# Performance work log

Hardware: AMD Instinct MI355X
Metric: run time of the kernel (lower is better)

## Reference

```python
import jax, jax.numpy as jnp
import numpy as np

H = 800          # config.param.hidden_size (768 bert + 32 pos)
BERT_H = 768
POS_DIM = 32
NHEAD = 8
DH = 100         # gat_nhidden; NHEAD*DH == H
GAT_LAYERS = 2
N_EVENTS = 66
N_ROLES = 122
EPS = 0.1        # label smoothing
NEG_SLOPE = 0.2  # GATConv leaky_relu slope


def bilstm(x, Wih_f, Whh_f, b_f, Wih_b, Whh_b, b_b):
    """x: [B,T,D] -> [B,T,2H] (torch gate order i,f,g,o)."""
    def run(xs, Wih, Whh, b):
        B = xs.shape[1]; Hd = Whh.shape[1]
        def step(carry, xt):
            h, c = carry
            g = xt @ Wih.T + h @ Whh.T + b
            i, f, gg, o = jnp.split(g, 4, axis=-1)
            c = jax.nn.sigmoid(f) * c + jax.nn.sigmoid(i) * jnp.tanh(gg)
            h = jax.nn.sigmoid(o) * jnp.tanh(c)
            return (h, c), h
        init = (jnp.zeros((B, Hd), xs.dtype), jnp.zeros((B, Hd), xs.dtype))
        _, hs = jax.lax.scan(step, init, xs)
        return hs
    xt = jnp.swapaxes(x, 0, 1)                      # [T,B,D]
    hf = run(xt, Wih_f, Whh_f, b_f)
    hb = run(xt[::-1], Wih_b, Whh_b, b_b)[::-1]
    return jnp.swapaxes(jnp.concatenate([hf, hb], -1), 0, 1)


def gat_conv(x, src, dst, W, a_src, a_dst, bias):
    """PyG GATConv, concat heads, with self-loops. x:[n,H], src/dst:[E]."""
    n = x.shape[0]
    loops = jnp.arange(n)
    s = jnp.concatenate([src, loops])
    d = jnp.concatenate([dst, loops])
    h = (x @ W).reshape(n, NHEAD, DH)
    a_s = jnp.einsum('nhd,hd->nh', h, a_src)
    a_d = jnp.einsum('nhd,hd->nh', h, a_dst)
    e = jax.nn.leaky_relu(a_s[s] + a_d[d], NEG_SLOPE)              # [E,nh]
    m = jnp.full((n, NHEAD), -jnp.inf, x.dtype).at[d].max(e)       # segment max
    ex = jnp.exp(e - m[d])
    den = jnp.zeros((n, NHEAD), x.dtype).at[d].add(ex)
    alpha = ex / den[d]
    out = jnp.zeros((n, NHEAD, DH), x.dtype).at[d].add(alpha[..., None] * h[s])
    return out.reshape(n, NHEAD * DH) + bias


def label_smooth_ce(logits, target):
    c = logits.shape[-1]
    logp = jax.nn.log_softmax(logits, axis=-1)
    smooth = -logp.sum(-1)
    nll = -jnp.take_along_axis(logp, target[..., None], axis=-1)[..., 0]
    return smooth * EPS / c + (1.0 - EPS) * nll


def setup_inputs() -> dict:
    key = jax.random.key(0)
    ks = iter(jax.random.split(key, 32))
    B, S, E = 4, 128, 256
    std = 0.02
    inp = {}
    inp['bert_out'] = jax.random.normal(next(ks), (B, S + 1, BERT_H), jnp.float32)
    inp['pos_ids'] = jax.random.randint(next(ks), (B, S), 0, 31)
    inp['edge_src'] = jax.random.randint(next(ks), (B, E), 0, S)
    inp['edge_dst'] = jax.random.randint(next(ks), (B, E), 0, S)
    inp['start_labels'] = jax.random.randint(next(ks), (B, S, S), 0, N_EVENTS)
    inp['end_labels'] = jax.random.randint(next(ks), (B, S, S), 0, N_EVENTS)
    # parameters
    inp['pos_table'] = std * jax.random.normal(next(ks), (31, POS_DIM), jnp.float32)
    for sfx in ('f', 'b'):
        inp[f'Wih_{sfx}'] = std * jax.random.normal(next(ks), (4 * H, H), jnp.float32)
        inp[f'Whh_{sfx}'] = std * jax.random.normal(next(ks), (4 * H, H), jnp.float32)
        inp[f'bl_{sfx}'] = jnp.zeros((4 * H,), jnp.float32)
    inp['lstm_fc_W'] = std * jax.random.normal(next(ks), (2 * H, H), jnp.float32)
    inp['lstm_fc_b'] = jnp.zeros((H,), jnp.float32)
    inp['table_W'] = std * jax.random.normal(next(ks), (2 * H, H), jnp.float32)
    inp['table_b'] = jnp.zeros((H,), jnp.float32)
    inp['gat_W'] = std * jax.random.normal(next(ks), (H, NHEAD * DH), jnp.float32)
    inp['gat_asrc'] = std * jax.random.normal(next(ks), (NHEAD, DH), jnp.float32)
    inp['gat_adst'] = std * jax.random.normal(next(ks), (NHEAD, DH), jnp.float32)
    inp['gat_bias'] = jnp.zeros((NHEAD * DH,), jnp.float32)
    inp['trig_W'] = std * jax.random.normal(next(ks), (H, N_EVENTS), jnp.float32)
    inp['trig_b'] = jnp.zeros((N_EVENTS,), jnp.float32)
    inp['rs_W'] = std * jax.random.normal(next(ks), (H, N_ROLES), jnp.float32)
    inp['rs_b'] = jnp.zeros((N_ROLES,), jnp.float32)
    inp['re_W'] = std * jax.random.normal(next(ks), (H, N_ROLES), jnp.float32)
    inp['re_b'] = jnp.zeros((N_ROLES,), jnp.float32)
    return inp


def reference(bert_out, pos_ids, edge_src, edge_dst, start_labels, end_labels,
              pos_table, Wih_f, Whh_f, bl_f, Wih_b, Whh_b, bl_b,
              lstm_fc_W, lstm_fc_b, table_W, table_b,
              gat_W, gat_asrc, gat_adst, gat_bias,
              trig_W, trig_b, rs_W, rs_b, re_W, re_b):
    B, S = pos_ids.shape
    # POS embedding, prepend zero vector for [CLS] position
    pos_emb = pos_table[pos_ids]                                   # [B,S,32]
    pos_emb = jnp.concatenate(
        [jnp.zeros((B, 1, POS_DIM), bert_out.dtype), pos_emb], axis=1)
    x = jnp.concatenate([bert_out, pos_emb], axis=-1)              # [B,S+1,800]
    lstm_out = bilstm(x, Wih_f, Whh_f, bl_f, Wih_b, Whh_b, bl_b)   # [B,S+1,1600]
    x = x + jax.nn.relu(lstm_out @ lstm_fc_W + lstm_fc_b)
    x = x[:, 1:, :]                                                # drop CLS -> [B,S,800]

    # per-sample residual GAT stack (eval mode: dropout is identity)
    def gat_stack(xi, si, di):
        for _ in range(GAT_LAYERS):
            xi = xi + jax.nn.relu(gat_conv(xi, si, di, gat_W, gat_asrc, gat_adst, gat_bias))
        return xi
    x = jax.vmap(gat_stack)(x, edge_src, edge_dst)                 # [B,S,800]

    # pairwise table: cat(x_i, x_j) -> fc -> gelu
    x1 = jnp.broadcast_to(x[:, :, None, :], (B, S, S, H))
    x2 = jnp.broadcast_to(x[:, None, :, :], (B, S, S, H))
    s_tab = jax.nn.gelu(jnp.concatenate([x1, x2], -1) @ table_W + table_b)  # [B,S,S,800]

    eye = jnp.eye(S, dtype=start_labels.dtype)
    trig_mask = eye                                                # [S,S]
    arg_mask = 1 - eye
    trig_maskf = trig_mask.astype(s_tab.dtype)
    arg_maskf = arg_mask.astype(s_tab.dtype)

    trig_logits = s_tab @ trig_W + trig_b                          # [B,S,S,66]
    arg1_logits = s_tab @ rs_W + rs_b                              # [B,S,S,122]
    arg2_logits = s_tab @ re_W + re_b

    def masked_mean(loss, maskf):
        return (loss * maskf).sum((1, 2)) / maskf.sum()

    l1 = masked_mean(label_smooth_ce(trig_logits, start_labels * trig_mask), trig_maskf)
    l2 = masked_mean(label_smooth_ce(arg1_logits, start_labels * arg_mask), arg_maskf)
    l3 = masked_mean(label_smooth_ce(arg2_logits, end_labels * arg_mask), arg_maskf)
    total_loss = (l1 + l2 + l3).sum()

    trig_pred = jnp.argmax(trig_logits, -1)
    a1_pred = jnp.argmax(arg1_logits + jnp.swapaxes(arg1_logits, 1, 2), -1)
    a2_pred = jnp.argmax(arg2_logits + jnp.swapaxes(arg2_logits, 1, 2), -1)
    results1 = trig_pred * trig_mask + a1_pred * arg_mask
    results2 = trig_pred * trig_mask + a2_pred * arg_mask
    return total_loss, results1, results2
```

## Files before the change

### kernel.cpp

```cpp
#include <hip/hip_runtime.h>
#include <hip/hip_bf16.h>

#define B4 4
#define S128 128
#define T129 129
#define H800 800
#define E256 256
#define NE 66
#define NR 122
#define DPW 8
#define NWGD 100

typedef float f32x4 __attribute__((ext_vector_type(4)));

#define HB_ROW 900

__device__ __forceinline__ float gelu_f(float x) {
    float t = 0.7978845608028654f * (x + 0.044715f * x * x * x);
    float e = __expf(2.f * t);
    float th = 1.f - 2.f / (e + 1.f);
    return 0.5f * x * (1.f + th);
}

__device__ __forceinline__ float embed_at(const float* __restrict__ bert,
                                          const int* __restrict__ pids,
                                          const float* __restrict__ ptab,
                                          int m, int c)
{
    if (c < 768) return bert[(size_t)m * 768 + c];
    int t = m % T129, b = m / T129;
    if (t == 0) return 0.f;
    return ptab[pids[b * S128 + t - 1] * 32 + (c - 768)];
}

template<int AMODE, int BTRANS, int EPI>
__global__ __launch_bounds__(256) void k_gemm(const float* __restrict__ A, const float* __restrict__ Bm,
                                              const float* __restrict__ bias, const float* __restrict__ res,
                                              float* __restrict__ C, int M, int N, int K)
{
    __shared__ float As[16][68];
    __shared__ float Bs[16][68];
    int m0 = blockIdx.x * 64, n0 = blockIdx.y * 64;
    int tid = threadIdx.x;
    int tm = tid & 15, tn = tid >> 4;
    int kkA = tid & 15, mmb = tid >> 4;
    int nnB = (tid & 15) * 4, kkB = tid >> 4;
    float acc[4][4] = {};
    float aP[4], bP[4];

    #pragma unroll
    for (int q = 0; q < 4; q++) {
        int m = m0 + mmb + q * 16;
        float v = 0.f;
        if (m < M) {
            int row = (AMODE == 1) ? (m + (m >> 7) + 1) : m;
            v = A[(size_t)row * K + kkA];
        }
        aP[q] = v;
    }
    if (BTRANS == 0) {
        int n = n0 + nnB;
        if (n + 3 < N) {
            float4 bv = *(const float4*)&Bm[(size_t)kkB * N + n];
            bP[0] = bv.x; bP[1] = bv.y; bP[2] = bv.z; bP[3] = bv.w;
        } else {
            #pragma unroll
            for (int q = 0; q < 4; q++)
                bP[q] = (n + q < N) ? Bm[(size_t)kkB * N + n + q] : 0.f;
        }
    } else {
        #pragma unroll
        for (int q = 0; q < 4; q++) {
            int n = n0 + mmb + q * 16;
            bP[q] = (n < N) ? Bm[(size_t)n * K + kkA] : 0.f;
        }
    }

    for (int k0 = 0; k0 < K; k0 += 16) {
        float aC[4], bC[4];
        #pragma unroll
        for (int q = 0; q < 4; q++) { aC[q] = aP[q]; bC[q] = bP[q]; }

        int kn = (k0 + 16 < K) ? (k0 + 16) : 0;
        #pragma unroll
        for (int q = 0; q < 4; q++) {
            int m = m0 + mmb + q * 16;
            float v = 0.f;
            if (m < M) {
                int row = (AMODE == 1) ? (m + (m >> 7) + 1) : m;
                v = A[(size_t)row * K + kn + kkA];
            }
            aP[q] = v;
        }
        if (BTRANS == 0) {
            int n = n0 + nnB;
            if (n + 3 < N) {
                float4 bv = *(const float4*)&Bm[(size_t)(kn + kkB) * N + n];
                bP[0] = bv.x; bP[1] = bv.y; bP[2] = bv.z; bP[3] = bv.w;
            } else {
                #pragma unroll
                for (int q = 0; q < 4; q++)
                    bP[q] = (n + q < N) ? Bm[(size_t)(kn + kkB) * N + n + q] : 0.f;
            }
        } else {
            #pragma unroll
            for (int q = 0; q < 4; q++) {
                int n = n0 + mmb + q * 16;
                bP[q] = (n < N) ? Bm[(size_t)n * K + kn + kkA] : 0.f;
            }
        }

        #pragma unroll
        for (int q = 0; q < 4; q++)
            As[kkA][mmb + q * 16] = aC[q];
        if (BTRANS == 0) {
            Bs[kkB][nnB + 0] = bC[0]; Bs[kkB][nnB + 1] = bC[1];
            Bs[kkB][nnB + 2] = bC[2]; Bs[kkB][nnB + 3] = bC[3];
        } else {
            #pragma unroll
            for (int q = 0; q < 4; q++)
                Bs[kkA][mmb + q * 16] = bC[q];
        }
        __syncthreads();
        #pragma unroll
        for (int kk = 0; kk < 16; kk++) {
            float4 a = *(const float4*)&As[kk][tm * 4];
            float4 bb = *(const float4*)&Bs[kk][tn * 4];
            float av[4] = {a.x, a.y, a.z, a.w};
            float bv[4] = {bb.x, bb.y, bb.z, bb.w};
            #pragma unroll
            for (int xx = 0; xx < 4; xx++)
                #pragma unroll
                for (int yy = 0; yy < 4; yy++)
                    acc[xx][yy] += av[xx] * bv[yy];
        }
        __syncthreads();
    }
    #pragma unroll
    for (int xx = 0; xx < 4; xx++) {
        int m = m0 + tm * 4 + xx;
        if (m >= M) continue;
        #pragma unroll
        for (int yy = 0; yy < 4; yy++) {
            int n = n0 + tn * 4 + yy;
            if (n >= N) continue;
            float v = acc[xx][yy];
            if (bias) v += bias[n];
            if (EPI == 1) v = res[(size_t)m * N + n] + fmaxf(v, 0.f);
            C[(size_t)m * N + n] = v;
        }
    }
}

__global__ __launch_bounds__(256) void k_gemm_wih(const float* __restrict__ bert,
                                                  const int* __restrict__ pids,
                                                  const float* __restrict__ ptab,
                                                  const float* __restrict__ Wf, const float* __restrict__ Wb,
                                                  const float* __restrict__ bf, const float* __restrict__ bb_,
                                                  float* __restrict__ C)
{
    __shared__ float As[16][68];
    __shared__ float Bs[16][68];
    const int M = 516, K = 800, N = 6400;
    int m0 = blockIdx.x * 64, n0 = blockIdx.y * 64;
    const float* W  = (n0 < 3200) ? Wf : Wb;
    const float* bi = (n0 < 3200) ? bf : bb_;
    int nb = (n0 < 3200) ? n0 : (n0 - 3200);
    int tid = threadIdx.x;
    int tm = tid & 15, tn = tid >> 4;
    int kk_s = tid & 15, mmb = tid >> 4;
    int mrow[4]; int pofs[4]; bool mok[4];
    #pragma unroll
    for (int q = 0; q < 4; q++) {
        int m = m0 + mmb + q * 16;
        mrow[q] = m;
        mok[q] = m < M;
        int t = m % T129, b = m / T129;
        pofs[q] = (mok[q] && t > 0) ? pids[b * S128 + t - 1] * 32 : -1;
    }
    float acc[4][4] = {};
    float aP[4], bP[4];

    #pragma unroll
    for (int q = 0; q < 4; q++) {
        float v = 0.f;
        if (mok[q]) {
            if (kk_s < 768) v = bert[(size_t)mrow[q] * 768 + kk_s];
            else            v = (pofs[q] < 0) ? 0.f : ptab[pofs[q] + kk_s - 768];
        }
        aP[q] = v;
    }
    #pragma unroll
    for (int q = 0; q < 4; q++)
        bP[q] = W[(size_t)(nb + mmb + q * 16) * K + kk_s];

    for (int k0 = 0; k0 < K; k0 += 16) {
        float aC[4], bC[4];
        #pragma unroll
        for (int q = 0; q < 4; q++) { aC[q] = aP[q]; bC[q] = bP[q]; }

        int kn = (k0 + 16 < K) ? (k0 + 16) : 0;
        {
            int c = kn + kk_s;
            #pragma unroll
            for (int q = 0; q < 4; q++) {
                float v = 0.f;
                if (mok[q]) {
                    if (c < 768) v = bert[(size_t)mrow[q] * 768 + c];
                    else         v = (pofs[q] < 0) ? 0.f : ptab[pofs[q] + c - 768];
                }
                aP[q] = v;
            }
        }
        #pragma unroll
        for (int q = 0; q < 4; q++)
            bP[q] = W[(size_t)(nb + mmb + q * 16) * K + kn + kk_s];

        #pragma unroll
        for (int q = 0; q < 4; q++)
            As[kk_s][mmb + q * 16] = aC[q];
        #pragma unroll
        for (int q = 0; q < 4; q++)
            Bs[kk_s][mmb + q * 16] = bC[q];
        __syncthreads();
        #pragma unroll
        for (int kk = 0; kk < 16; kk++) {
            float4 a = *(const float4*)&As[kk][tm * 4];
            float4 bb = *(const float4*)&Bs[kk][tn * 4];
            float av[4] = {a.x, a.y, a.z, a.w};
            float bv[4] = {bb.x, bb.y, bb.z, bb.w};
            #pragma unroll
            for (int xx = 0; xx < 4; xx++)
                #pragma unroll
                for (int yy = 0; yy < 4; yy++)
                    acc[xx][yy] += av[xx] * bv[yy];
        }
        __syncthreads();
    }
    #pragma unroll
    for (int xx = 0; xx < 4; xx++) {
        int m = m0 + tm * 4 + xx;
        if (m >= M) continue;
        #pragma unroll
        for (int yy = 0; yy < 4; yy++) {
            int n = n0 + tn * 4 + yy;
            C[(size_t)m * N + n] = acc[xx][yy] + bi[nb + (n - n0)];
        }
    }
}

__global__ __launch_bounds__(256) void k_gemm_fc(const float* __restrict__ A, const float* __restrict__ Bm,
                                                 const float* __restrict__ bias,
                                                 const float* __restrict__ bert, const int* __restrict__ pids,
                                                 const float* __restrict__ ptab, float* __restrict__ C)
{
    __shared__ float As[16][68];
    __shared__ float Bs[16][68];
    const int M = 516, N = 800, K = 1600;
    int m0 = blockIdx.x * 64, n0 = blockIdx.y * 64;
    int tid = threadIdx.x;
    int tm = tid & 15, tn = tid >> 4;
    int kkA = tid & 15, mmb = tid >> 4;
    int nnB = (tid & 15) * 4, kkB = tid >> 4;
    float acc[4][4] = {};
    float aP[4], bP[4];

    #pragma unroll
    for (int q = 0; q < 4; q++) {
        int m = m0 + mmb + q * 16;
        aP[q] = (m < M) ? A[(size_t)m * K + kkA] : 0.f;
    }
    {
        int n = n0 + nnB;
        if (n + 3 < N) {
            float4 bv = *(const float4*)&Bm[(size_t)kkB * N + n];
            bP[0] = bv.x; bP[1] = bv.y; bP[2] = bv.z; bP[3] = bv.w;
        } else {
            #pragma unroll
            for (int q = 0; q < 4; q++)
                bP[q] = (n + q < N) ? Bm[(size_t)kkB * N + n + q] : 0.f;
        }
    }

    for (int k0 = 0; k0 < K; k0 += 16) {
        float aC[4], bC[4];
        #pragma unroll
        for (int q = 0; q < 4; q++) { aC[q] = aP[q]; bC[q] = bP[q]; }

        int kn = (k0 + 16 < K) ? (k0 + 16) : 0;
        #pragma unroll
        for (int q = 0; q < 4; q++) {
            int m = m0 + mmb + q * 16;
            aP[q] = (m < M) ? A[(size_t)m * K + kn + kkA] : 0.f;
        }
        {
            int n = n0 + nnB;
            if (n + 3 < N) {
                float4 bv = *(const float4*)&Bm[(size_t)(kn + kkB) * N + n];
                bP[0] = bv.x; bP[1] = bv.y; bP[2] = bv.z; bP[3] = bv.w;
            } else {
                #pragma unroll
                for (int q = 0; q < 4; q++)
                    bP[q] = (n + q < N) ? Bm[(size_t)(kn + kkB) * N + n + q] : 0.f;
            }
        }

        #pragma unroll
        for (int q = 0; q < 4; q++)
            As[kkA][mmb + q * 16] = aC[q];
        Bs[kkB][nnB + 0] = bC[0]; Bs[kkB][nnB + 1] = bC[1];
        Bs[kkB][nnB + 2] = bC[2]; Bs[kkB][nnB + 3] = bC[3];
        __syncthreads();
        #pragma unroll
        for (int kk = 0; kk < 16; kk++) {
            float4 a = *(const float4*)&As[kk][tm * 4];
            float4 bb = *(const float4*)&Bs[kk][tn * 4];
            float av[4] = {a.x, a.y, a.z, a.w};
            float bv[4] = {bb.x, bb.y, bb.z, bb.w};
            #pragma unroll
            for (int xx = 0; xx < 4; xx++)
                #pragma unroll
                for (int yy = 0; yy < 4; yy++)
                    acc[xx][yy] += av[xx] * bv[yy];
        }
        __syncthreads();
    }
    #pragma unroll
    for (int xx = 0; xx < 4; xx++) {
        int m = m0 + tm * 4 + xx;
        if (m >= M) continue;
        #pragma unroll
        for (int yy = 0; yy < 4; yy++) {
            int n = n0 + tn * 4 + yy;
            if (n >= N) continue;
            float v = fmaxf(acc[xx][yy] + bias[n], 0.f);
            C[(size_t)m * N + n] = embed_at(bert, pids, ptab, m, n) + v;
        }
    }
}

__global__ __launch_bounds__(256) void k_gemm_uv(const float* __restrict__ A, const float* __restrict__ tW,
                                                 const float* __restrict__ tb, float* __restrict__ C)
{
    __shared__ float As[16][68];
    __shared__ float Bs[16][68];
    const int M = 512, K = 800, N = 1600;
    int m0 = blockIdx.x * 64, n0 = blockIdx.y * 64;
    int tid = threadIdx.x;
    int tm = tid & 15, tn = tid >> 4;
    int kkA = tid & 15, mmb = tid >> 4;
    int nnB = (tid & 15) * 4, kkB = tid >> 4;
    float acc[4][4] = {};
    float aP[4], bP[4];

    #pragma unroll
    for (int q = 0; q < 4; q++)
        aP[q] = A[(size_t)(m0 + mmb + q * 16) * K + kkA];
    #pragma unroll
    for (int q = 0; q < 4; q++) {
        int n = n0 + nnB + q;
        bP[q] = (n < 800) ? tW[(size_t)kkB * 800 + n]
                          : tW[(size_t)(800 + kkB) * 800 + (n - 800)];
    }

    for (int k0 = 0; k0 < K; k0 += 16) {
        float aC[4], bC[4];
        #pragma unroll
        for (int q = 0; q < 4; q++) { aC[q] = aP[q]; bC[q] = bP[q]; }

        int kn = (k0 + 16 < K) ? (k0 + 16) : 0;
        #pragma unroll
        for (int q = 0; q < 4; q++)
            aP[q] = A[(size_t)(m0 + mmb + q * 16) * K + kn + kkA];
        #pragma unroll
        for (int q = 0; q < 4; q++) {
            int n = n0 + nnB + q;
            bP[q] = (n < 800) ? tW[(size_t)(kn + kkB) * 800 + n]
                              : tW[(size_t)(800 + kn + kkB) * 800 + (n - 800)];
        }

        #pragma unroll
        for (int q = 0; q < 4; q++)
            As[kkA][mmb + q * 16] = aC[q];
        #pragma unroll
        for (int q = 0; q < 4; q++)
            Bs[kkB][nnB + q] = bC[q];
        __syncthreads();
        #pragma unroll
        for (int kk = 0; kk < 16; kk++) {
            float4 a = *(const float4*)&As[kk][tm * 4];
            float4 bb = *(const float4*)&Bs[kk][tn * 4];
            float av[4] = {a.x, a.y, a.z, a.w};
            float bv[4] = {bb.x, bb.y, bb.z, bb.w};
            #pragma unroll
            for (int xx = 0; xx < 4; xx++)
                #pragma unroll
                for (int yy = 0; yy < 4; yy++)
                    acc[xx][yy] += av[xx] * bv[yy];
        }
        __syncthreads();
    }
    #pragma unroll
    for (int xx = 0; xx < 4; xx++) {
        int m = m0 + tm * 4 + xx;
        #pragma unroll
        for (int yy = 0; yy < 4; yy++) {
            int n = n0 + tn * 4 + yy;
            float v = acc[xx][yy];
            if (n < 800) v += tb[n];
            C[(size_t)m * N + n] = v;
        }
    }
}

__global__ __launch_bounds__(256) void k_lstm(const float* __restrict__ xW,
                                              const float* __restrict__ Whhf, const float* __restrict__ Whhb,
                                              float* __restrict__ lstm, float* __restrict__ hpk)
{
    __shared__ float hb[4][HB_ROW];
    __shared__ float gsum[25][32][4];
    __shared__ float gg[128];
    int wg = blockIdx.x;
    int dir = wg >= NWGD ? 1 : 0;
    int wgd = dir ? wg - NWGD : wg;
    const float* Whh = dir ? Whhb : Whhf;
    const float* xWd = xW + dir * 3200;
    int tid = threadIdx.x;
    bool dotth = tid < 200;
    int d = tid & 7, sl = tid >> 3;
    int k0 = sl * 32;
    int rb = tid & 3, rd = (tid >> 2) & 7, rg = tid >> 5;
    int lane = tid & 63;

    float wreg[4][32];
    if (dotth) {
        #pragma unroll
        for (int g = 0; g < 4; g++) {
            const float* wp = Whh + (size_t)(g * 800 + wgd * DPW + d) * 800 + k0;
            #pragma unroll
            for (int q = 0; q < 32; q += 4)
                *(float4*)&wreg[g][q] = *(const float4*)&wp[q];
        }
    }
    for (int i = tid; i < 4 * HB_ROW; i += 256) (&hb[0][0])[i] = 0.f;
    __syncthreads();

    float cst = 0.f;

    for (int step = 0; step < 129; step++) {
        int t = dir ? (128 - step) : step;
        float xq = 0.f;
        if (tid < 128)
            xq = xWd[(size_t)(rb * T129 + t) * 6400 + rg * 800 + wgd * DPW + rd];
        if (step > 0) {
            int tprev = dir ? (t + 1) : (t - 1);
            if (tid < 200) {
                const f32x4* pb = (const f32x4*)(hpk + (size_t)(dir * 129 + tprev) * 3200);
                const f32x4* p0 = pb + tid;
                const f32x4* p1 = pb + tid + 200;
                const f32x4* p2 = pb + tid + 400;
                const f32x4* p3 = pb + tid + 600;
                f32x4 v0, v1, v2, v3;
                long long iters = 0;
                for (;;) {
                    asm volatile(
                        "global_load_dwordx4 %0, %4, off sc0 sc1\n\t"
                        "global_load_dwordx4 %1, %5, off sc0 sc1\n\t"
                        "global_load_dwordx4 %2, %6, off sc0 sc1\n\t"
                        "global_load_dwordx4 %3, %7, off sc0 sc1\n\t"
                        "s_waitcnt vmcnt(0)"
                        : "=&v"(v0), "=&v"(v1), "=&v"(v2), "=&v"(v3)
                        : "v"(p0), "v"(p1), "v"(p2), "v"(p3)
                        : "memory");
                    bool ok = fabsf(v0.x) < 1.5f && fabsf(v0.y) < 1.5f &&
                              fabsf(v0.z) < 1.5f && fabsf(v0.w) < 1.5f &&
                              fabsf(v1.x) < 1.5f && fabsf(v1.y) < 1.5f &&
                              fabsf(v1.z) < 1.5f && fabsf(v1.w) < 1.5f &&
                              fabsf(v2.x) < 1.5f && fabsf(v2.y) < 1.5f &&
                              fabsf(v2.z) < 1.5f && fabsf(v2.w) < 1.5f &&
                              fabsf(v3.x) < 1.5f && fabsf(v3.y) < 1.5f &&
                              fabsf(v3.z) < 1.5f && fabsf(v3.w) < 1.5f;
                    if (ok) break;
                    if (++iters > 20000000LL) break;
                }
                {
                    int s0 = tid;
                    int p_ = (s0 >> 3) * 8 + (s0 & 1) * 4;
                    ((f32x4*)&hb[0][0])[((s0 & 7) >> 1) * 225 + (p_ >> 5) * 9 + ((p_ & 31) >> 2)] = v0;
                }
                {
                    int s1 = tid + 200;
                    int p_ = (s1 >> 3) * 8 + (s1 & 1) * 4;
                    ((f32x4*)&hb[0][0])[((s1 & 7) >> 1) * 225 + (p_ >> 5) * 9 + ((p_ & 31) >> 2)] = v1;
                }
                {
                    int s2 = tid + 400;
                    int p_ = (s2 >> 3) * 8 + (s2 & 1) * 4;
                    ((f32x4*)&hb[0][0])[((s2 & 7) >> 1) * 225 + (p_ >> 5) * 9 + ((p_ & 31) >> 2)] = v2;
                }
                {
                    int s3 = tid + 600;
                    int p_ = (s3 >> 3) * 8 + (s3 & 1) * 4;
                    ((f32x4*)&hb[0][0])[((s3 & 7) >> 1) * 225 + (p_ >> 5) * 9 + ((p_ & 31) >> 2)] = v3;
                }
            }
            __syncthreads();
        }
        if (dotth) {
            float a[4][4] = {};
            #pragma unroll
            for (int b = 0; b < 4; b++) {
                const float* hrow = &hb[b][0];
                #pragma unroll
                for (int q = 0; q < 32; q += 4) {
                    float4 h = *(const float4*)&hrow[sl * 36 + q];
                    #pragma unroll
                    for (int g = 0; g < 4; g++)
                        a[g][b] += wreg[g][q] * h.x + wreg[g][q + 1] * h.y
                                 + wreg[g][q + 2] * h.z + wreg[g][q + 3] * h.w;
                }
            }
            #pragma unroll
            for (int g = 0; g < 4; g++)
                *(float4*)&gsum[sl][g * 8 + d][0] = make_float4(a[g][0], a[g][1], a[g][2], a[g][3]);
        }
        __syncthreads();
        if (tid < 128) {
            float s = xq;
            #pragma unroll
            for (int ss = 0; ss < 25; ss++) s += gsum[ss][rg * 8 + rd][rb];
            gg[tid] = s;
        }
        __syncthreads();
        float hv = 0.f;
        if (tid < 32) {
            int dd = tid & 7, bb2 = tid >> 3;
            float gi = gg[(0 << 5) | (dd << 2) | bb2];
            float gf = gg[(1 << 5) | (dd << 2) | bb2];
            float gG = gg[(2 << 5) | (dd << 2) | bb2];
            float go = gg[(3 << 5) | (dd << 2) | bb2];
            float si = 1.f / (1.f + __expf(-gi));
            float sf = 1.f / (1.f + __expf(-gf));
            float so = 1.f / (1.f + __expf(-go));
            cst = sf * cst + si * tanhf(gG);
            hv = so * tanhf(cst);
        }
        if (tid < 64) {
            int src = (lane & 7) * 4;
            f32x4 o;
            o.x = __shfl(hv, src + 0, 64);
            o.y = __shfl(hv, src + 1, 64);
            o.z = __shfl(hv, src + 2, 64);
            o.w = __shfl(hv, src + 3, 64);
            if (lane < 8) {
                float* pp = hpk + ((size_t)(dir * 129 + t) * 100 + wgd) * 32 + lane * 4;
                asm volatile("global_store_dwordx4 %0, %1, off sc0 sc1"
                             :: "v"((f32x4*)pp), "v"(o) : "memory");
            }
            if (lane < 8) {
                int bb = lane >> 1, half = lane & 1;
                float* ap = lstm + (size_t)((bb * T129 + t) * 1600) + dir * 800 + wgd * DPW + half * 4;
                asm volatile("global_store_dwordx4 %0, %1, off sc0 sc1"
                             :: "v"((f32x4*)ap), "v"(o) : "memory");
            }
        }
    }
}

template<int RESMODE>
__global__ __launch_bounds__(512) void k_gat_fused(const int* __restrict__ esrc, const int* __restrict__ edst,
                                                   const float* __restrict__ h1,
                                                   const float* __restrict__ asrc, const float* __restrict__ adst,
                                                   const float* __restrict__ gbias,
                                                   const float* __restrict__ res, float* __restrict__ out)
{
    __shared__ int se[384], de[384];
    __shared__ float asl[128], adl[128], ml[128], dl_[128];
    int bh = blockIdx.x;
    int b = bh >> 3, h = bh & 7;
    int t = threadIdx.x;
    if (t < 384) {
        if (t < E256) { se[t] = esrc[b * E256 + t]; de[t] = edst[b * E256 + t]; }
        else          { se[t] = t - E256;           de[t] = t - E256; }
    }
    int node = t >> 2, ch = t & 3;
    int dd0 = ch * 25;
    {
        const float* hp = h1 + (size_t)(b * S128 + node) * H800 + h * 100 + dd0;
        const float* ap = asrc + h * 100 + dd0;
        const float* dp = adst + h * 100 + dd0;
        float s1 = 0.f, s2 = 0.f;
        #pragma unroll
        for (int q = 0; q < 25; q++) { float hv = hp[q]; s1 += hv * ap[q]; s2 += hv * dp[q]; }
        s1 += __shfl_xor(s1, 1, 64); s1 += __shfl_xor(s1, 2, 64);
        s2 += __shfl_xor(s2, 1, 64); s2 += __shfl_xor(s2, 2, 64);
        if (ch == 0) { asl[node] = s1; adl[node] = s2; }
    }
    __syncthreads();
    if (t < 128) {
        float myad = adl[t];
        float m = -3.4e38f;
        for (int e = 0; e < 384; e++)
            if (de[e] == t) {
                float sc = asl[se[e]] + myad;
                sc = (sc > 0.f) ? sc : 0.2f * sc;
                m = fmaxf(m, sc);
            }
        float den = 0.f;
        for (int e = 0; e < 384; e++)
            if (de[e] == t) {
                float sc = asl[se[e]] + myad;
                sc = (sc > 0.f) ? sc : 0.2f * sc;
                den += __expf(sc - m);
            }
        ml[t] = m; dl_[t] = den;
    }
    __syncthreads();
    float acc[25] = {};
    float myad = adl[node], mym = ml[node];
    for (int e = 0; e < 384; e++) {
        if (de[e] == node) {
            int s = se[e];
            float sc = asl[s] + myad;
            sc = (sc > 0.f) ? sc : 0.2f * sc;
            float w = __expf(sc - mym);
            const float* hp = h1 + (size_t)(b * S128 + s) * H800 + h * 100 + dd0;
            #pragma unroll
            for (int q = 0; q < 25; q++) acc[q] += w * hp[q];
        }
    }
    float inv = 1.f / dl_[node];
    int n = b * S128 + node;
    size_t rrow = (RESMODE == 1) ? (size_t)(n + b + 1) * H800 : (size_t)n * H800;
    #pragma unroll
    for (int q = 0; q < 25; q++) {
        int col = h * 100 + dd0 + q;
        float v = acc[q] * inv + gbias[col];
        out[(size_t)n * H800 + col] = res[rrow + col] + fmaxf(v, 0.f);
    }
}

__global__ __launch_bounds__(64) void k_trig(const float* __restrict__ uv,
                                             const float* __restrict__ W, const float* __restrict__ bias,
                                             const int* __restrict__ labels, float* __restrict__ d_out)
{
    __shared__ float s[800];
    __shared__ float lg[66];
    int bi = blockIdx.x;
    int i = bi & 127;
    int l = threadIdx.x;
    const float* ur = uv + (size_t)bi * 1600;
    const float* vr = ur + 800;
    for (int k = l; k < 800; k += 64) s[k] = gelu_f(ur[k] + vr[k]);
    __syncthreads();
    float a0 = 0.f, a1 = 0.f;
    bool has2 = (l < 2);
    for (int k = 0; k < 800; k++) {
        float sv = s[k];
        a0 += sv * W[k * NE + l];
        if (has2) a1 += sv * W[k * NE + 64 + l];
    }
    lg[l] = a0 + bias[l];
    if (has2) lg[64 + l] = a1 + bias[64 + l];
    __syncthreads();
    if (l == 0) {
        float m = lg[0];
        for (int c = 1; c < NE; c++) m = fmaxf(m, lg[c]);
        float se = 0.f, sl = 0.f, bv = lg[0];
        int am = 0;
        for (int c = 0; c < NE; c++) {
            se += __expf(lg[c] - m);
            sl += lg[c];
            if (lg[c] > bv) { bv = lg[c]; am = c; }
        }
        float lse = m + __logf(se);
        int tgt = labels[(size_t)bi * S128 + i];
        float ce = (0.1f / NE) * (NE * lse - sl) + 0.9f * (lse - lg[tgt]);
        atomicAdd(d_out, ce * (1.f / 128.f));
        int r = bi * S128 + i;
        d_out[1 + r] = (float)am;
        d_out[1 + 65536 + r] = (float)am;
    }
}

__global__ __launch_bounds__(256) void k_logits2(const float* __restrict__ uvb,
                                                 const float* __restrict__ rsW, const float* __restrict__ rsb,
                                                 const float* __restrict__ reW, const float* __restrict__ reb,
                                                 float* __restrict__ L)
{
    __shared__ float As[16][68];
    __shared__ float Bs[16][256];
    int bi = blockIdx.y;
    const float* base = uvb + (size_t)bi * 128 * 1600;
    float* Lb = L + (size_t)bi * 16384 * 256;
    int il = blockIdx.x >> 1;
    int j0 = (blockIdx.x & 1) * 64;
    const float* urow = base + (size_t)il * 1600;
    int tid = threadIdx.x;
    int tm = tid & 7, tn = tid >> 3;
    float acc[8][8] = {};
    int ct = tid;
    int hc = (ct < 128) ? ct : (ct - 128);
    const float* Wp = (ct < 128) ? rsW : reW;
    bool cok = hc < NR;
    int kk = tid & 15, rrb = tid >> 4;

    float u_pf = urow[kk];
    float v_pf[4];
    #pragma unroll
    for (int q = 0; q < 4; q++)
        v_pf[q] = base[(size_t)(j0 + rrb + q * 16) * 1600 + 800 + kk];
    float w_pf[16];
    #pragma unroll
    for (int kk2 = 0; kk2 < 16; kk2++)
        w_pf[kk2] = cok ? Wp[(size_t)kk2 * NR + hc] : 0.f;

    for (int k0 = 0; k0 < 800; k0 += 16) {
        float u_cur = u_pf;
        float v_cur[4];
        #pragma unroll
        for (int q = 0; q < 4; q++) v_cur[q] = v_pf[q];
        float w_cur[16];
        #pragma unroll
        for (int kk2 = 0; kk2 < 16; kk2++) w_cur[kk2] = w_pf[kk2];

        int kn = (k0 + 16 < 800) ? (k0 + 16) : 0;
        u_pf = urow[kn + kk];
        #pragma unroll
        for (int q = 0; q < 4; q++)
            v_pf[q] = base[(size_t)(j0 + rrb + q * 16) * 1600 + 800 + kn + kk];
        #pragma unroll
        for (int kk2 = 0; kk2 < 16; kk2++)
            w_pf[kk2] = cok ? Wp[(size_t)(kn + kk2) * NR + hc] : 0.f;

        #pragma unroll
        for (int q = 0; q < 4; q++)
            As[kk][rrb + q * 16] = gelu_f(u_cur + v_cur[q]);
        #pragma unroll
        for (int kk2 = 0; kk2 < 16; kk2++)
            Bs[kk2][ct] = w_cur[kk2];
        __syncthreads();
        #pragma unroll
        for (int kki = 0; kki < 16; kki++) {
            float4 a0 = *(const float4*)&As[kki][tm * 8];
            float4 a1 = *(const float4*)&As[kki][tm * 8 + 4];
            float4 b0 = *(const float4*)&Bs[kki][tn * 8];
            float4 b1 = *(const float4*)&Bs[kki][tn * 8 + 4];
            float av[8] = {a0.x, a0.y, a0.z, a0.w, a1.x, a1.y, a1.z, a1.w};
            float bv[8] = {b0.x, b0.y, b0.z, b0.w, b1.x, b1.y, b1.z, b1.w};
            #pragma unroll
            for (int xx = 0; xx < 8; xx++)
                #pragma unroll
                for (int yy = 0; yy < 8; yy++)
                    acc[xx][yy] += av[xx] * bv[yy];
        }
        __syncthreads();
    }
    int head = tn >> 4;
    const float* bp = head ? reb : rsb;
    #pragma unroll
    for (int xx = 0; xx < 8; xx++) {
        int r = il * S128 + j0 + tm * 8 + xx;
        float* Lr = Lb + (size_t)r * 256 + tn * 8;
        #pragma unroll
        for (int hf = 0; hf < 2; hf++) {
            int c = (tn * 8 + hf * 4) & 127;
            if (c + 3 < NR) {
                float4 o = make_float4(acc[xx][hf*4+0] + bp[c+0], acc[xx][hf*4+1] + bp[c+1],
                                       acc[xx][hf*4+2] + bp[c+2], acc[xx][hf*4+3] + bp[c+3]);
                *(float4*)(Lr + hf * 4) = o;
            } else {
                #pragma unroll
                for (int q = 0; q < 4; q++)
                    if (c + q < NR) Lr[hf * 4 + q] = acc[xx][hf*4+q] + bp[c+q];
            }
        }
    }
}

__global__ __launch_bounds__(256) void k_loss2(const float* __restrict__ L,
                                               const int* __restrict__ lab0, const int* __restrict__ lab1,
                                               float* __restrict__ res0, float* __restrict__ res1,
                                               float* __restrict__ lossptr)
{
    __shared__ float wsum[4];
    int wv = threadIdx.x >> 6, l = threadIdx.x & 63;
    int rr = blockIdx.x * 4 + wv;
    int bi = rr >> 14;
    int r = rr & 16383;
    int i = r >> 7, j = r & 127;
    size_t bioff = (size_t)bi * 16384;
    float ces = 0.f;
    if (i != j) {
        const float* row  = L + (bioff + r) * 256;
        const float* prow = L + (bioff + ((j << 7) | i)) * 256;
        bool v2 = (l < NR - 64);
        #pragma unroll
        for (int hd = 0; hd < 2; hd++) {
            const float* rw = row + hd * 128;
            const float* pw = prow + hd * 128;
            float x1 = rw[l];
            float x2 = v2 ? rw[l + 64] : -3.4e38f;
            float m = fmaxf(x1, x2);
            #pragma unroll
            for (int s = 32; s; s >>= 1) m = fmaxf(m, __shfl_xor(m, s, 64));
            float se = __expf(x1 - m) + (v2 ? __expf(x2 - m) : 0.f);
            float sl = x1 + (v2 ? x2 : 0.f);
            #pragma unroll
            for (int s = 32; s; s >>= 1) { se += __shfl_xor(se, s, 64); sl += __shfl_xor(sl, s, 64); }
            float lse = m + __logf(se);
            int tgt = (hd ? lab1 : lab0)[bioff + r];
            float lt = rw[tgt];
            ces += (0.1f / NR) * (NR * lse - sl) + 0.9f * (lse - lt);
            float y1 = x1 + pw[l];
            float y2 = v2 ? (x2 + pw[l + 64]) : -3.4e38f;
            float bv; int bidx;
            if (y2 > y1) { bv = y2; bidx = l + 64; } else { bv = y1; bidx = l; }
            #pragma unroll
            for (int s = 32; s; s >>= 1) {
                float ov = __shfl_xor(bv, s, 64);
                int oi = __shfl_xor(bidx, s, 64);
                if (ov > bv || (ov == bv && oi < bidx)) { bv = ov; bidx = oi; }
            }
            if (l == 0) (hd ? res1 : res0)[bioff + r] = (float)bidx;
        }
    }
    if (l == 0) wsum[wv] = ces;
    __syncthreads();
    if (threadIdx.x == 0) {
        float s = (wsum[0] + wsum[1] + wsum[2] + wsum[3]) * (1.f / 16256.f);
        atomicAdd(lossptr, s);
    }
}

extern "C" void kernel_launch(void* const* d_in, const int* in_sizes, int n_in,
                              void* d_out, int out_size, void* d_ws, size_t ws_size,
                              hipStream_t stream)
{
    (void)in_sizes; (void)n_in; (void)out_size;
    const float* bert  = (const float*)d_in[0];
    const int*   pids  = (const int*)d_in[1];
    const int*   esrc  = (const int*)d_in[2];
    const int*   edst  = (const int*)d_in[3];
    const int*   slab  = (const int*)d_in[4];
    const int*   elab  = (const int*)d_in[5];
    const float* ptab  = (const float*)d_in[6];
    const float* Wih_f = (const float*)d_in[7];
    const float* Whh_f = (const float*)d_in[8];
    const float* bl_f  = (const float*)d_in[9];
    const float* Wih_b = (const float*)d_in[10];
    const float* Whh_b = (const float*)d_in[11];
    const float* bl_b  = (const float*)d_in[12];
    const float* fcW   = (const float*)d_in[13];
    const float* fcb   = (const float*)d_in[14];
    const float* tW    = (const float*)d_in[15];
    const float* tb    = (const float*)d_in[16];
    const float* gatW  = (const float*)d_in[17];
    const float* asrc  = (const float*)d_in[18];
    const float* adst  = (const float*)d_in[19];
    const float* gbias = (const float*)d_in[20];
    const float* trigW = (const float*)d_in[21];
    const float* trigb = (const float*)d_in[22];
    const float* rsW   = (const float*)d_in[23];
    const float* rsb   = (const float*)d_in[24];
    const float* reW   = (const float*)d_in[25];
    const float* reb   = (const float*)d_in[26];
    float* out = (float*)d_out;

    float* ws = (float*)d_ws;
    size_t off = 0;
    auto alloc = [&](size_t n) { float* p = ws + off; off += (n + 255) & ~(size_t)255; return p; };
    float* uv    = alloc((size_t)512 * 1600);
    float* R     = ws + off;
    size_t roff = 0;
    auto ralloc = [&](size_t n) { float* p = R + roff; roff += (n + 255) & ~(size_t)255; return p; };
    float* xW   = ralloc((size_t)516 * 6400);
    float* lstm = ralloc((size_t)516 * 1600);
    float* xg   = ralloc(516 * 800);
    float* h1   = ralloc(512 * 800);
    float* g1   = ralloc(512 * 800);
    float* g2   = ralloc(512 * 800);
    float* hpk  = ralloc((size_t)2 * 129 * 100 * 32);
    float* Lbuf = R;

    hipMemsetAsync(d_out, 0, 4, stream);
    hipMemsetAsync(hpk, 0x7F, (size_t)2 * 129 * 100 * 32 * sizeof(float), stream);

    k_gemm_wih<<<dim3(9, 100), 256, 0, stream>>>(bert, pids, ptab, Wih_f, Wih_b, bl_f, bl_b, xW);

    k_lstm<<<2 * NWGD, 256, 0, stream>>>(xW, Whh_f, Whh_b, lstm, hpk);

    k_gemm_fc<<<dim3(9, 13), 256, 0, stream>>>(lstm, fcW, fcb, bert, pids, ptab, xg);

    k_gemm<1, 0, 0><<<dim3(8, 13), 256, 0, stream>>>(xg, gatW, nullptr, nullptr, h1, 512, 800, 800);
    k_gat_fused<1><<<32, 512, 0, stream>>>(esrc, edst, h1, asrc, adst, gbias, xg, g1);
    k_gemm<0, 0, 0><<<dim3(8, 13), 256, 0, stream>>>(g1, gatW, nullptr, nullptr, h1, 512, 800, 800);
    k_gat_fused<0><<<32, 512, 0, stream>>>(esrc, edst, h1, asrc, adst, gbias, g1, g2);

    k_gemm_uv<<<dim3(8, 25), 256, 0, stream>>>(g2, tW, tb, uv);

    k_trig<<<512, 64, 0, stream>>>(uv, trigW, trigb, slab, out);

    size_t need4 = (off + (size_t)4 * 16384 * 256) * sizeof(float);
    if (ws_size >= need4) {
        k_logits2<<<dim3(256, 4), 256, 0, stream>>>(uv, rsW, rsb, reW, reb, Lbuf);
        k_loss2<<<16384, 256, 0, stream>>>(Lbuf, slab, elab,
                                           out + 1, out + 1 + 65536, out);
    } else {
        for (int bp = 0; bp < 2; bp++) {
            k_logits2<<<dim3(256, 2), 256, 0, stream>>>(uv + (size_t)bp * 2 * 128 * 1600,
                                                        rsW, rsb, reW, reb, Lbuf);
            k_loss2<<<8192, 256, 0, stream>>>(Lbuf,
                                              slab + (size_t)bp * 2 * 16384, elab + (size_t)bp * 2 * 16384,
                                              out + 1 + (size_t)bp * 2 * 16384,
                                              out + 1 + 65536 + (size_t)bp * 2 * 16384, out);
        }
    }
}
```

Before: 1.927 ms.

## Double-buffer GELU A tile and use per-wave weight tiles in logits2

```diff
diff --git a/kernel.cpp b/kernel.cpp
--- a/kernel.cpp
+++ b/kernel.cpp
@@ -688,8 +688,8 @@
                                                  const float* __restrict__ reW, const float* __restrict__ reb,
                                                  float* __restrict__ L)
 {
-    __shared__ float As[16][68];
-    __shared__ float Bs[16][256];
+    __shared__ float As[2][16][68];
+    __shared__ float Bs[4][16][68];
     int bi = blockIdx.y;
     const float* base = uvb + (size_t)bi * 128 * 1600;
     float* Lb = L + (size_t)bi * 16384 * 256;
@@ -697,62 +697,67 @@
     int j0 = (blockIdx.x & 1) * 64;
     const float* urow = base + (size_t)il * 1600;
     int tid = threadIdx.x;
+    int wv = tid >> 6, lane = tid & 63;
     int tm = tid & 7, tn = tid >> 3;
+    int cln = (tn & 7) * 8;
     float acc[8][8] = {};
-    int ct = tid;
-    int hc = (ct < 128) ? ct : (ct - 128);
-    const float* Wp = (ct < 128) ? rsW : reW;
+    int hc = (tid < 128) ? tid : (tid - 128);
+    const float* Wp = (tid < 128) ? rsW : reW;
     bool cok = hc < NR;
     int kk = tid & 15, rrb = tid >> 4;
 
-    float u_pf = urow[kk];
-    float v_pf[4];
+    float u0 = urow[kk];
+    float v0q[4];
     #pragma unroll
     for (int q = 0; q < 4; q++)
-        v_pf[q] = base[(size_t)(j0 + rrb + q * 16) * 1600 + 800 + kk];
-    float w_pf[16];
+        v0q[q] = base[(size_t)(j0 + rrb + q * 16) * 1600 + 800 + kk];
+    float wP[16];
     #pragma unroll
     for (int kk2 = 0; kk2 < 16; kk2++)
-        w_pf[kk2] = cok ? Wp[(size_t)kk2 * NR + hc] : 0.f;
-
-    for (int k0 = 0; k0 < 800; k0 += 16) {
-        float u_cur = u_pf;
-        float v_cur[4];
-        #pragma unroll
-        for (int q = 0; q < 4; q++) v_cur[q] = v_pf[q];
-        float w_cur[16];
-        #pragma unroll
-        for (int kk2 = 0; kk2 < 16; kk2++) w_cur[kk2] = w_pf[kk2];
-
-        int kn = (k0 + 16 < 800) ? (k0 + 16) : 0;
-        u_pf = urow[kn + kk];
+        wP[kk2] = cok ? Wp[(size_t)kk2 * NR + hc] : 0.f;
+    float uP = urow[16 + kk];
+    float vP[4];
+    #pragma unroll
+    for (int q = 0; q < 4; q++)
+        vP[q] = base[(size_t)(j0 + rrb + q * 16) * 1600 + 800 + 16 + kk];
+
+    #pragma unroll
+    for (int q = 0; q < 4; q++)
+        As[0][kk][rrb + q * 16] = gelu_f(u0 + v0q[q]);
+    __syncthreads();
+
+    for (int c = 0; c < 50; ++c) {
+        #pragma unroll
+        for (int kk2 = 0; kk2 < 16; kk2++)
+            Bs[wv][kk2][lane] = wP[kk2];
         #pragma unroll
         for (int q = 0; q < 4; q++)
-            v_pf[q] = base[(size_t)(j0 + rrb + q * 16) * 1600 + 800 + kn + kk];
+            As[(c + 1) & 1][kk][rrb + q * 16] = gelu_f(uP + vP[q]);
+
+        int k1 = (c + 1 < 50) ? (c + 1) * 16 : 0;
+        int k2 = (c + 2 < 50) ? (c + 2) * 16 : 0;
         #pragma unroll
         for (int kk2 = 0; kk2 < 16; kk2++)
-            w_pf[kk2] = cok ? Wp[(size_t)(kn + kk2) * NR + hc] : 0.f;
-
+            wP[kk2] = cok ? Wp[(size_t)(k1 + kk2) * NR + hc] : 0.f;
+        uP = urow[k2 + kk];
         #pragma unroll
         for (int q = 0; q < 4; q++)
-            As[kk][rrb + q * 16] = gelu_f(u_cur + v_cur[q]);
-        #pragma unroll
-        for (int kk2 = 0; kk2 < 16; kk2++)
-            Bs[kk2][ct] = w_cur[kk2];
-        __syncthreads();
+            vP[q] = base[(size_t)(j0 + rrb + q * 16) * 1600 + 800 + k2 + kk];
+
+        const float (*Ac)[68] = As[c & 1];
         #pragma unroll
         for (int kki = 0; kki < 16; kki++) {
-            float4 a0 = *(const float4*)&As[kki][tm * 8];
-            float4 a1 = *(const float4*)&As[kki][tm * 8 + 4];
-            float4 b0 = *(const float4*)&Bs[kki][tn * 8];
-            float4 b1 = *(const float4*)&Bs[kki][tn * 8 + 4];
+            float4 a0 = *(const float4*)&Ac[kki][tm * 8];
+            float4 a1 = *(const float4*)&Ac[kki][tm * 8 + 4];
+            float4 b0 = *(const float4*)&Bs[wv][kki][cln];
+            float4 b1 = *(const float4*)&Bs[wv][kki][cln + 4];
             float av[8] = {a0.x, a0.y, a0.z, a0.w, a1.x, a1.y, a1.z, a1.w};
-            float bv[8] = {b0.x, b0.y, b0.z, b0.w, b1.x, b1.y, b1.z, b1.w};
+            float bvv[8] = {b0.x, b0.y, b0.z, b0.w, b1.x, b1.y, b1.z, b1.w};
             #pragma unroll
             for (int xx = 0; xx < 8; xx++)
                 #pragma unroll
                 for (int yy = 0; yy < 8; yy++)
-                    acc[xx][yy] += av[xx] * bv[yy];
+                    acc[xx][yy] += av[xx] * bvv[yy];
         }
         __syncthreads();
     }
```

Result: no change. 1.908 ms, median of 2 (-1.0%).
